# Optimization experiments

Measured on AMD Instinct MI355X. Metric: run time of the kernel, lower is better.

## Reference

```python
import jax, jax.numpy as jnp
import numpy as np
import math

B, LQ, LK = 1024, 1, 1024
LQD, SQD, H = 256, 128, 2
HD = SQD // H  # 64
EPS = 1e-6


def _ln(x, g, b):
    mu = x.mean(-1, keepdims=True)
    var = ((x - mu) ** 2).mean(-1, keepdims=True)
    return (x - mu) / jnp.sqrt(var + EPS) * g + b


def setup_inputs() -> dict:
    key = jax.random.key(0)
    ks = jax.random.split(key, 16)
    w = lambda k, s: jax.random.normal(k, s, jnp.float32) * 0.02
    return {
        "q_feats": jax.random.normal(ks[0], (B, LQ, LQD), jnp.float32),
        "k_feats": jax.random.normal(ks[1], (B, LK, SQD), jnp.float32),
        "msk": jax.random.randint(ks[2], (B, LK), 0, 2).astype(jnp.int32),
        "ln1_g": jnp.ones(LQD), "ln1_b": jnp.zeros(LQD),
        "W1": w(ks[3], (LQD, SQD)), "b1": jnp.zeros(SQD),
        "lnq_g": jnp.ones(SQD), "lnq_b": jnp.zeros(SQD),
        "lnk_g": jnp.ones(SQD), "lnk_b": jnp.zeros(SQD),
        "Wq": w(ks[4], (SQD, SQD)), "bq": jnp.zeros(SQD),
        "Wk": w(ks[5], (SQD, SQD)), "bk": jnp.zeros(SQD),
        "Wv": w(ks[6], (SQD, SQD)), "bv": jnp.zeros(SQD),
        "Wo": w(ks[7], (SQD, SQD)), "bo": jnp.zeros(SQD),
        "scale_w": jax.random.uniform(ks[8], (SQD,), jnp.float32, 0.01, 2.0),
        "ln2_g": jnp.ones(SQD), "ln2_b": jnp.zeros(SQD),
        "W2": w(ks[9], (SQD, LQD)), "b2": jnp.zeros(LQD),
    }


def reference(q_feats, k_feats, msk, ln1_g, ln1_b, W1, b1, lnq_g, lnq_b,
              lnk_g, lnk_b, Wq, bq, Wk, bk, Wv, bv, Wo, bo, scale_w,
              ln2_g, ln2_b, W2, b2):
    gelu = lambda x: jax.nn.gelu(x, approximate=False)
    # q_block1: LN -> Linear -> GELU (dropout = identity in eval)
    q_atten = gelu(_ln(q_feats, ln1_g, ln1_b) @ W1 + b1)  # [B,LQ,SQD]
    kv_in = _ln(k_feats, lnk_g, lnk_b)                     # [B,LK,SQD]
    q_in = _ln(q_atten, lnq_g, lnq_b)
    # masked self-attention
    qh = (q_in @ Wq + bq).reshape(B, LQ, H, HD).transpose(0, 2, 1, 3)
    kh = (kv_in @ Wk + bk).reshape(B, LK, H, HD).transpose(0, 2, 1, 3)
    vh = (kv_in @ Wv + bv).reshape(B, LK, H, HD).transpose(0, 2, 1, 3)
    scores = jnp.einsum('bhqd,bhkd->bhqk', qh, kh) / math.sqrt(HD)
    m = msk.astype(scores.dtype)[:, None, None, :]  # [B,1,1,LK]
    scores = jnp.where(m == 0, -1e9, scores * m)
    attn = jax.nn.softmax(scores, axis=-1)
    ctx = jnp.einsum('bhqk,bhkd->bhqd', attn, vh)
    ctx = ctx.transpose(0, 2, 1, 3).reshape(B, LQ, SQD)
    attn_out = gelu(ctx @ Wo + bo)
    q_atten = q_atten + attn_out
    # scaled broadcast residual into k_feats
    scaled = jnp.swapaxes(q_atten * scale_w, 0, 1)         # [LQ,B,SQD]
    k_out = k_feats + jnp.tile(scaled, (B, 1, 1))          # [B,B,SQD]
    # q_block2
    q_out = q_feats + gelu(_ln(q_atten, ln2_g, ln2_b) @ W2 + b2)
    return (q_out, k_out)
```

## Files before the change

kernel.cpp:

```cpp
#include <hip/hip_runtime.h>
#include <math.h>

#define B_    1024
#define LK_   1024
#define LQD_  256
#define SQD_  128
#define EPSLN 1e-6f
#define LOG2E 1.4426950408889634f

__device__ __forceinline__ float gelu_exact(float x) {
    return 0.5f * x * (1.0f + erff(x * 0.70710678118654752f));
}

__global__ __launch_bounds__(256, 4)
void fused_joint_kernel(
    const float* __restrict__ q_feats, const float* __restrict__ k_feats,
    const int*   __restrict__ msk,
    const float* __restrict__ ln1_g, const float* __restrict__ ln1_b,
    const float* __restrict__ W1,    const float* __restrict__ b1,
    const float* __restrict__ lnq_g, const float* __restrict__ lnq_b,
    const float* __restrict__ lnk_g, const float* __restrict__ lnk_b,
    const float* __restrict__ Wq,    const float* __restrict__ bq,
    const float* __restrict__ Wk,    const float* __restrict__ bk,
    const float* __restrict__ Wv,    const float* __restrict__ bv,
    const float* __restrict__ Wo,    const float* __restrict__ bo,
    const float* __restrict__ scale_w,
    const float* __restrict__ ln2_g, const float* __restrict__ ln2_b,
    const float* __restrict__ W2,    const float* __restrict__ b2,
    float* __restrict__ q_out, float* __restrict__ k_out)
{
    const int b    = blockIdx.x;
    const int tid  = threadIdx.x;
    const int wave = tid >> 6;
    const int lane = tid & 63;

    __shared__ float s_qn[256];
    __shared__ float s_q1[128];
    __shared__ float s_qi[128];
    __shared__ float s_qh[128];
    __shared__ float s_u[2][128];
    __shared__ float s_c[2];
    __shared__ float s_red[8];
    __shared__ int   s_idx[4][256];
    __shared__ float s_w[4][2][128];
    __shared__ float s_ml[4][2][2];
    __shared__ float s_wn[2][128];
    __shared__ float s_ctx[128];
    __shared__ float s_qa[128];
    __shared__ float s_qn2[128];
    __shared__ float s_sc[128];

    float x = q_feats[b * LQD_ + tid];
    float rs = x, rss = x * x;
    #pragma unroll
    for (int o = 32; o >= 1; o >>= 1) { rs += __shfl_xor(rs, o); rss += __shfl_xor(rss, o); }
    if (lane == 0) { s_red[wave * 2] = rs; s_red[wave * 2 + 1] = rss; }
    __syncthreads();
    {
        float sum  = s_red[0] + s_red[2] + s_red[4] + s_red[6];
        float ssum = s_red[1] + s_red[3] + s_red[5] + s_red[7];
        float mu   = sum * (1.0f / 256.0f);
        float var  = ssum * (1.0f / 256.0f) - mu * mu;
        float rstd = rsqrtf(var + EPSLN);
        s_qn[tid] = (x - mu) * rstd * ln1_g[tid] + ln1_b[tid];
    }
    __syncthreads();

    if (tid < 128) {
        float acc = b1[tid];
        #pragma unroll 4
        for (int c = 0; c < 256; ++c) acc = fmaf(s_qn[c], W1[c * 128 + tid], acc);
        s_q1[tid] = gelu_exact(acc);
    }
    __syncthreads();

    float v1 = (tid < 128) ? s_q1[tid] : 0.0f;
    rs = v1; rss = v1 * v1;
    #pragma unroll
    for (int o = 32; o >= 1; o >>= 1) { rs += __shfl_xor(rs, o); rss += __shfl_xor(rss, o); }
    __syncthreads();
    if (lane == 0) { s_red[wave * 2] = rs; s_red[wave * 2 + 1] = rss; }
    __syncthreads();
    {
        float sum  = s_red[0] + s_red[2] + s_red[4] + s_red[6];
        float ssum = s_red[1] + s_red[3] + s_red[5] + s_red[7];
        float mu   = sum * (1.0f / 128.0f);
        float var  = ssum * (1.0f / 128.0f) - mu * mu;
        float rstd = rsqrtf(var + EPSLN);
        if (tid < 128) s_qi[tid] = (v1 - mu) * rstd * lnq_g[tid] + lnq_b[tid];
    }
    __syncthreads();

    if (tid < 128) {
        float acc = bq[tid];
        #pragma unroll 4
        for (int c = 0; c < 128; ++c) acc = fmaf(s_qi[c], Wq[c * 128 + tid], acc);
        s_qh[tid] = acc;
    }
    __syncthreads();

    const float SCL = 0.125f * LOG2E;
    if (tid < 128) {
        float a0 = 0.f, a1 = 0.f;
        #pragma unroll 4
        for (int e = 0; e < 64; ++e) {
            a0 = fmaf(Wk[tid * 128 + e],      s_qh[e],      a0);
            a1 = fmaf(Wk[tid * 128 + 64 + e], s_qh[64 + e], a1);
        }
        s_u[0][tid] = a0 * SCL;
        s_u[1][tid] = a1 * SCL;
    }
    if (tid == 0) { float a = 0.f; for (int e = 0; e < 64; ++e) a = fmaf(bk[e],      s_qh[e],      a); s_c[0] = a * SCL; }
    if (tid == 1) { float a = 0.f; for (int e = 0; e < 64; ++e) a = fmaf(bk[64 + e], s_qh[64 + e], a); s_c[1] = a * SCL; }

    const int* mrow = msk + b * LK_;
    int cnt = 0;
    #pragma unroll
    for (int i = 0; i < 4; ++i) {
        int r = (wave << 8) + (i << 6) + lane;
        int mk = mrow[r];
        unsigned long long bal = __ballot(mk != 0);
        int pre = __popcll(bal & ((1ull << lane) - 1ull));
        if (mk) s_idx[wave][cnt + pre] = r;
        cnt += __popcll(bal);
    }
    __syncthreads();

    const int  c0i = lane * 2, c1i = lane * 2 + 1;
    const float g0  = lnk_g[c0i], g1  = lnk_g[c1i];
    const float hb0 = lnk_b[c0i], hb1 = lnk_b[c1i];
    const float u00 = s_u[0][c0i], u01 = s_u[0][c1i];
    const float u10 = s_u[1][c0i], u11 = s_u[1][c1i];
    const float cc0 = s_c[0],      cc1 = s_c[1];

    const float gu00 = g0 * u00, gu01 = g1 * u01;
    const float gu10 = g0 * u10, gu11 = g1 * u11;
    float sgu0 = gu00 + gu01;
    float sgu1 = gu10 + gu11;
    float dd0  = fmaf(hb0, u00, hb1 * u01);
    float dd1  = fmaf(hb0, u10, hb1 * u11);
    #pragma unroll
    for (int o = 32; o >= 1; o >>= 1) {
        sgu0 += __shfl_xor(sgu0, o); sgu1 += __shfl_xor(sgu1, o);
        dd0  += __shfl_xor(dd0,  o); dd1  += __shfl_xor(dd1,  o);
    }
    const float d0 = dd0 + cc0, d1 = dd1 + cc1;

    const float2* kf2 = (const float2*)(k_feats) + (size_t)b * (LK_ * (SQD_ / 2));

    float m0 = -1e30f, l0 = 0.f, w00 = 0.f, w01 = 0.f;
    float m1 = -1e30f, l1 = 0.f, w10 = 0.f, w11 = 0.f;

    #define ROW_STEP(xx, valid)                                               \
    {                                                                         \
        float a_  = xx.x + xx.y;                                              \
        float q_  = fmaf(xx.x, xx.x, xx.y * xx.y);                            \
        float p0_ = fmaf(xx.x, gu00, xx.y * gu01);                            \
        float p1_ = fmaf(xx.x, gu10, xx.y * gu11);                            \
        _Pragma("unroll")                                                     \
        for (int o_ = 32; o_ >= 1; o_ >>= 1) {                                \
            a_  += __shfl_xor(a_,  o_); q_  += __shfl_xor(q_,  o_);           \
            p0_ += __shfl_xor(p0_, o_); p1_ += __shfl_xor(p1_, o_);           \
        }                                                                     \
        if (valid) {                                                          \
            float mu_   = a_ * (1.f / 128.f);                                 \
            float var_  = q_ * (1.f / 128.f) - mu_ * mu_;                     \
            float rstd_ = rsqrtf(var_ + EPSLN);                               \
            float sc0_  = fmaf(rstd_, p0_ - mu_ * sgu0, d0);                  \
            float sc1_  = fmaf(rstd_, p1_ - mu_ * sgu1, d1);                  \
            float kv0_  = fmaf((xx.x - mu_) * rstd_, g0, hb0);                \
            float kv1_  = fmaf((xx.y - mu_) * rstd_, g1, hb1);                \
            float mn0_  = fmaxf(m0, sc0_);                                    \
            float cr0_  = exp2f(m0 - mn0_);                                   \
            float pp0_  = exp2f(sc0_ - mn0_);                                 \
            m0 = mn0_; l0 = fmaf(l0, cr0_, pp0_);                             \
            w00 = fmaf(w00, cr0_, pp0_ * kv0_);                               \
            w01 = fmaf(w01, cr0_, pp0_ * kv1_);                               \
            float mn1_  = fmaxf(m1, sc1_);                                    \
            float cr1_  = exp2f(m1 - mn1_);                                   \
            float pp1_  = exp2f(sc1_ - mn1_);                                 \
            m1 = mn1_; l1 = fmaf(l1, cr1_, pp1_);                             \
            w10 = fmaf(w10, cr1_, pp1_ * kv0_);                               \
            w11 = fmaf(w11, cr1_, pp1_ * kv1_);                               \
        }                                                                     \
    }

    float2 xr0 = make_float2(0.f, 0.f), xr1 = xr0, xr2 = xr0, xr3 = xr0;
    if (0 < cnt) xr0 = kf2[s_idx[wave][0] * 64 + lane];
    if (1 < cnt) xr1 = kf2[s_idx[wave][1] * 64 + lane];
    if (2 < cnt) xr2 = kf2[s_idx[wave][2] * 64 + lane];
    if (3 < cnt) xr3 = kf2[s_idx[wave][3] * 64 + lane];

    for (int t = 0; t < cnt; t += 4) {
        float2 xn0 = make_float2(0.f, 0.f), xn1 = xn0, xn2 = xn0, xn3 = xn0;
        if (t + 4 < cnt) xn0 = kf2[s_idx[wave][t + 4] * 64 + lane];
        if (t + 5 < cnt) xn1 = kf2[s_idx[wave][t + 5] * 64 + lane];
        if (t + 6 < cnt) xn2 = kf2[s_idx[wave][t + 6] * 64 + lane];
        if (t + 7 < cnt) xn3 = kf2[s_idx[wave][t + 7] * 64 + lane];

        ROW_STEP(xr0, true);
        ROW_STEP(xr1, (t + 1) < cnt);
        ROW_STEP(xr2, (t + 2) < cnt);
        ROW_STEP(xr3, (t + 3) < cnt);

        xr0 = xn0; xr1 = xn1; xr2 = xn2; xr3 = xn3;
    }
    #undef ROW_STEP

    s_w[wave][0][c0i] = w00; s_w[wave][0][c1i] = w01;
    s_w[wave][1][c0i] = w10; s_w[wave][1][c1i] = w11;
    if (lane == 0) {
        s_ml[wave][0][0] = m0; s_ml[wave][0][1] = l0;
        s_ml[wave][1][0] = m1; s_ml[wave][1][1] = l1;
    }
    __syncthreads();

    if (tid < 128) {
        #pragma unroll
        for (int h = 0; h < 2; ++h) {
            float mg = fmaxf(fmaxf(s_ml[0][h][0], s_ml[1][h][0]),
                             fmaxf(s_ml[2][h][0], s_ml[3][h][0]));
            float lt = 0.f, wt = 0.f;
            #pragma unroll
            for (int wv = 0; wv < 4; ++wv) {
                float e = exp2f(s_ml[wv][h][0] - mg);
                lt += s_ml[wv][h][1] * e;
                wt += s_w[wv][h][tid] * e;
            }
            s_wn[h][tid] = wt / lt;
        }
    }
    __syncthreads();

    if (tid < 128) {
        int h = tid >> 6;
        float acc = bv[tid];
        #pragma unroll 4
        for (int c = 0; c < 128; ++c) acc = fmaf(s_wn[h][c], Wv[c * 128 + tid], acc);
        s_ctx[tid] = acc;
    }
    __syncthreads();

    if (tid < 128) {
        float acc = bo[tid];
        #pragma unroll 4
        for (int c = 0; c < 128; ++c) acc = fmaf(s_ctx[c], Wo[c * 128 + tid], acc);
        float qa = s_q1[tid] + gelu_exact(acc);
        s_qa[tid] = qa;
        s_sc[tid] = qa * scale_w[tid];
    }
    __syncthreads();

    float v2 = (tid < 128) ? s_qa[tid] : 0.0f;
    rs = v2; rss = v2 * v2;
    #pragma unroll
    for (int o = 32; o >= 1; o >>= 1) { rs += __shfl_xor(rs, o); rss += __shfl_xor(rss, o); }
    __syncthreads();
    if (lane == 0) { s_red[wave * 2] = rs; s_red[wave * 2 + 1] = rss; }
    __syncthreads();
    {
        float sum  = s_red[0] + s_red[2] + s_red[4] + s_red[6];
        float ssum = s_red[1] + s_red[3] + s_red[5] + s_red[7];
        float mu   = sum * (1.0f / 128.0f);
        float var  = ssum * (1.0f / 128.0f) - mu * mu;
        float rstd = rsqrtf(var + EPSLN);
        if (tid < 128) s_qn2[tid] = (v2 - mu) * rstd * ln2_g[tid] + ln2_b[tid];
    }
    __syncthreads();

    {
        float acc = b2[tid];
        #pragma unroll 4
        for (int c = 0; c < 128; ++c) acc = fmaf(s_qn2[c], W2[c * 256 + tid], acc);
        q_out[b * LQD_ + tid] = q_feats[b * LQD_ + tid] + gelu_exact(acc);
    }

    {
        const int c4 = tid & 31;
        const int r0 = tid >> 5;
        const float4 sv = ((const float4*)s_sc)[c4];
        const size_t colbase = (size_t)b * 32 + c4;
        const float4* __restrict__ kin4  = (const float4*)k_feats;
        float4*       __restrict__ kout4 = (float4*)k_out;
        #pragma unroll 4
        for (int b2 = r0; b2 < B_; b2 += 8) {
            size_t o = (size_t)b2 * (LK_ * 32) + colbase;
            float4 kx = kin4[o];
            float4 ov = make_float4(kx.x + sv.x, kx.y + sv.y, kx.z + sv.z, kx.w + sv.w);
            kout4[o] = ov;
        }
    }
}

extern "C" void kernel_launch(void* const* d_in, const int* in_sizes, int n_in,
                              void* d_out, int out_size, void* d_ws, size_t ws_size,
                              hipStream_t stream)
{
    (void)in_sizes; (void)n_in; (void)out_size; (void)d_ws; (void)ws_size;
    const float* q_feats = (const float*)d_in[0];
    const float* k_feats = (const float*)d_in[1];
    const int*   msk     = (const int*)d_in[2];
    const float* ln1_g   = (const float*)d_in[3];
    const float* ln1_b   = (const float*)d_in[4];
    const float* W1      = (const float*)d_in[5];
    const float* b1      = (const float*)d_in[6];
    const float* lnq_g   = (const float*)d_in[7];
    const float* lnq_b   = (const float*)d_in[8];
    const float* lnk_g   = (const float*)d_in[9];
    const float* lnk_b   = (const float*)d_in[10];
    const float* Wq      = (const float*)d_in[11];
    const float* bq      = (const float*)d_in[12];
    const float* Wk      = (const float*)d_in[13];
    const float* bk      = (const float*)d_in[14];
    const float* Wv      = (const float*)d_in[15];
    const float* bv      = (const float*)d_in[16];
    const float* Wo      = (const float*)d_in[17];
    const float* bo      = (const float*)d_in[18];
    const float* scale_w = (const float*)d_in[19];
    const float* ln2_g   = (const float*)d_in[20];
    const float* ln2_b   = (const float*)d_in[21];
    const float* W2      = (const float*)d_in[22];
    const float* b2      = (const float*)d_in[23];

    float* q_out = (float*)d_out;
    float* k_out = (float*)d_out + (size_t)B_ * LQD_;

    fused_joint_kernel<<<B_, 256, 0, stream>>>(
        q_feats, k_feats, msk, ln1_g, ln1_b, W1, b1, lnq_g, lnq_b,
        lnk_g, lnk_b, Wq, bq, Wk, bk, Wv, bv, Wo, bo, scale_w,
        ln2_g, ln2_b, W2, b2, q_out, k_out);
}
```

Measured before the change: 387.0 us.

## Stage masked key rows through LDS tiles and batch the online softmax per tile

The per-row attention loop, which used a full 64-lane shuffle reduction for every key row, is replaced by a tiled scheme. Each wave loads 16 masked rows into a padded LDS tile with float4 loads. Quarter-wave partial dot products compute the per-row LayerNorm stats and scores with only two shuffle levels, and the running max is updated once per tile before the weighted accumulation. Shared-memory buffers are aliased to fit the larger tile, mask indices shrink to ushort, and the k_out broadcast store now uses nontemporal stores. This adds LDS traffic and code complexity in exchange for fewer cross-lane reductions and exp calls per row.

```diff
diff --git a/kernel.cpp b/kernel.cpp
--- a/kernel.cpp
+++ b/kernel.cpp
@@ -7,6 +7,13 @@
 #define SQD_  128
 #define EPSLN 1e-6f
 #define LOG2E 1.4426950408889634f
+
+#define TROWS 16
+#define TF4   33
+#define WREGF4 (TROWS * TF4)
+#define WREGF  (WREGF4 * 4)
+
+typedef float floatx4 __attribute__((ext_vector_type(4)));
 
 __device__ __forceinline__ float gelu_exact(float x) {
     return 0.5f * x * (1.0f + erff(x * 0.70710678118654752f));
@@ -34,21 +41,26 @@
     const int wave = tid >> 6;
     const int lane = tid & 63;
 
-    __shared__ float s_qn[256];
+    __shared__ float4 s_tile4[4 * WREGF4];
+    __shared__ float4 s_meta[4][TROWS];
+    __shared__ unsigned short s_idxm[4][256];
+    __shared__ __align__(16) float s_gu[2][128];
     __shared__ float s_q1[128];
-    __shared__ float s_qi[128];
-    __shared__ float s_qh[128];
-    __shared__ float s_u[2][128];
-    __shared__ float s_c[2];
+    __shared__ float s_sc[128];
     __shared__ float s_red[8];
-    __shared__ int   s_idx[4][256];
-    __shared__ float s_w[4][2][128];
     __shared__ float s_ml[4][2][2];
-    __shared__ float s_wn[2][128];
-    __shared__ float s_ctx[128];
-    __shared__ float s_qa[128];
-    __shared__ float s_qn2[128];
-    __shared__ float s_sc[128];
+
+    float* s_flat = (float*)s_tile4;
+    float* s_qn = s_flat;
+    float* s_qi = s_flat + 256;
+    float* s_qh = s_flat + 384;
+    float* s_u0 = s_flat + 512;
+    float* s_u1 = s_flat + 640;
+    float* s_c2 = s_flat + 768;
+    float* s_wn  = s_flat + 1024;
+    float* s_ctx = s_flat + 1280;
+    float* s_qa  = s_flat + 1408;
+    float* s_qn2 = s_flat + 1536;
 
     float x = q_feats[b * LQD_ + tid];
     float rs = x, rss = x * x;
@@ -107,11 +119,34 @@
             a0 = fmaf(Wk[tid * 128 + e],      s_qh[e],      a0);
             a1 = fmaf(Wk[tid * 128 + 64 + e], s_qh[64 + e], a1);
         }
-        s_u[0][tid] = a0 * SCL;
-        s_u[1][tid] = a1 * SCL;
-    }
-    if (tid == 0) { float a = 0.f; for (int e = 0; e < 64; ++e) a = fmaf(bk[e],      s_qh[e],      a); s_c[0] = a * SCL; }
-    if (tid == 1) { float a = 0.f; for (int e = 0; e < 64; ++e) a = fmaf(bk[64 + e], s_qh[64 + e], a); s_c[1] = a * SCL; }
+        s_u0[tid] = a0 * SCL;
+        s_u1[tid] = a1 * SCL;
+    }
+    if (tid == 0) { float a = 0.f; for (int e = 0; e < 64; ++e) a = fmaf(bk[e],      s_qh[e],      a); s_c2[0] = a * SCL; }
+    if (tid == 1) { float a = 0.f; for (int e = 0; e < 64; ++e) a = fmaf(bk[64 + e], s_qh[64 + e], a); s_c2[1] = a * SCL; }
+    __syncthreads();
+
+    const int  c0i = lane * 2, c1i = lane * 2 + 1;
+    const float g0  = lnk_g[c0i], g1  = lnk_g[c1i];
+    const float hb0 = lnk_b[c0i], hb1 = lnk_b[c1i];
+    const float u00 = s_u0[c0i], u01 = s_u0[c1i];
+    const float u10 = s_u1[c0i], u11 = s_u1[c1i];
+    const float cc0 = s_c2[0],   cc1 = s_c2[1];
+    if (tid < 128) {
+        float g = lnk_g[tid];
+        s_gu[0][tid] = s_u0[tid] * g;
+        s_gu[1][tid] = s_u1[tid] * g;
+    }
+    float sgu0 = fmaf(g0, u00, g1 * u01);
+    float sgu1 = fmaf(g0, u10, g1 * u11);
+    float dd0  = fmaf(hb0, u00, hb1 * u01);
+    float dd1  = fmaf(hb0, u10, hb1 * u11);
+    #pragma unroll
+    for (int o = 32; o >= 1; o >>= 1) {
+        sgu0 += __shfl_xor(sgu0, o); sgu1 += __shfl_xor(sgu1, o);
+        dd0  += __shfl_xor(dd0,  o); dd1  += __shfl_xor(dd1,  o);
+    }
+    const float d0 = dd0 + cc0, d1 = dd1 + cc1;
 
     const int* mrow = msk + b * LK_;
     int cnt = 0;
@@ -121,97 +156,124 @@
         int mk = mrow[r];
         unsigned long long bal = __ballot(mk != 0);
         int pre = __popcll(bal & ((1ull << lane) - 1ull));
-        if (mk) s_idx[wave][cnt + pre] = r;
+        if (mk) s_idxm[wave][cnt + pre] = (unsigned short)r;
         cnt += __popcll(bal);
     }
     __syncthreads();
 
-    const int  c0i = lane * 2, c1i = lane * 2 + 1;
-    const float g0  = lnk_g[c0i], g1  = lnk_g[c1i];
-    const float hb0 = lnk_b[c0i], hb1 = lnk_b[c1i];
-    const float u00 = s_u[0][c0i], u01 = s_u[0][c1i];
-    const float u10 = s_u[1][c0i], u11 = s_u[1][c1i];
-    const float cc0 = s_c[0],      cc1 = s_c[1];
-
-    const float gu00 = g0 * u00, gu01 = g1 * u01;
-    const float gu10 = g0 * u10, gu11 = g1 * u11;
-    float sgu0 = gu00 + gu01;
-    float sgu1 = gu10 + gu11;
-    float dd0  = fmaf(hb0, u00, hb1 * u01);
-    float dd1  = fmaf(hb0, u10, hb1 * u11);
-    #pragma unroll
-    for (int o = 32; o >= 1; o >>= 1) {
-        sgu0 += __shfl_xor(sgu0, o); sgu1 += __shfl_xor(sgu1, o);
-        dd0  += __shfl_xor(dd0,  o); dd1  += __shfl_xor(dd1,  o);
-    }
-    const float d0 = dd0 + cc0, d1 = dd1 + cc1;
-
-    const float2* kf2 = (const float2*)(k_feats) + (size_t)b * (LK_ * (SQD_ / 2));
+    float4* twave = s_tile4 + wave * WREGF4;
+    const float* twf = (const float*)twave;
+    const float4* kf4 = (const float4*)k_feats + (size_t)b * (LK_ * 32);
+    const float4* gu04 = (const float4*)s_gu[0];
+    const float4* gu14 = (const float4*)s_gu[1];
+    const int half  = lane >> 5;
+    const int chunk = lane & 31;
+    const int arow  = lane & 15;
+    const int aq    = lane >> 4;
 
     float m0 = -1e30f, l0 = 0.f, w00 = 0.f, w01 = 0.f;
     float m1 = -1e30f, l1 = 0.f, w10 = 0.f, w11 = 0.f;
 
-    #define ROW_STEP(xx, valid)                                               \
-    {                                                                         \
-        float a_  = xx.x + xx.y;                                              \
-        float q_  = fmaf(xx.x, xx.x, xx.y * xx.y);                            \
-        float p0_ = fmaf(xx.x, gu00, xx.y * gu01);                            \
-        float p1_ = fmaf(xx.x, gu10, xx.y * gu11);                            \
-        _Pragma("unroll")                                                     \
-        for (int o_ = 32; o_ >= 1; o_ >>= 1) {                                \
-            a_  += __shfl_xor(a_,  o_); q_  += __shfl_xor(q_,  o_);           \
-            p0_ += __shfl_xor(p0_, o_); p1_ += __shfl_xor(p1_, o_);           \
-        }                                                                     \
-        if (valid) {                                                          \
-            float mu_   = a_ * (1.f / 128.f);                                 \
-            float var_  = q_ * (1.f / 128.f) - mu_ * mu_;                     \
-            float rstd_ = rsqrtf(var_ + EPSLN);                               \
-            float sc0_  = fmaf(rstd_, p0_ - mu_ * sgu0, d0);                  \
-            float sc1_  = fmaf(rstd_, p1_ - mu_ * sgu1, d1);                  \
-            float kv0_  = fmaf((xx.x - mu_) * rstd_, g0, hb0);                \
-            float kv1_  = fmaf((xx.y - mu_) * rstd_, g1, hb1);                \
-            float mn0_  = fmaxf(m0, sc0_);                                    \
-            float cr0_  = exp2f(m0 - mn0_);                                   \
-            float pp0_  = exp2f(sc0_ - mn0_);                                 \
-            m0 = mn0_; l0 = fmaf(l0, cr0_, pp0_);                             \
-            w00 = fmaf(w00, cr0_, pp0_ * kv0_);                               \
-            w01 = fmaf(w01, cr0_, pp0_ * kv1_);                               \
-            float mn1_  = fmaxf(m1, sc1_);                                    \
-            float cr1_  = exp2f(m1 - mn1_);                                   \
-            float pp1_  = exp2f(sc1_ - mn1_);                                 \
-            m1 = mn1_; l1 = fmaf(l1, cr1_, pp1_);                             \
-            w10 = fmaf(w10, cr1_, pp1_ * kv0_);                               \
-            w11 = fmaf(w11, cr1_, pp1_ * kv1_);                               \
-        }                                                                     \
-    }
-
-    float2 xr0 = make_float2(0.f, 0.f), xr1 = xr0, xr2 = xr0, xr3 = xr0;
-    if (0 < cnt) xr0 = kf2[s_idx[wave][0] * 64 + lane];
-    if (1 < cnt) xr1 = kf2[s_idx[wave][1] * 64 + lane];
-    if (2 < cnt) xr2 = kf2[s_idx[wave][2] * 64 + lane];
-    if (3 < cnt) xr3 = kf2[s_idx[wave][3] * 64 + lane];
-
-    for (int t = 0; t < cnt; t += 4) {
-        float2 xn0 = make_float2(0.f, 0.f), xn1 = xn0, xn2 = xn0, xn3 = xn0;
-        if (t + 4 < cnt) xn0 = kf2[s_idx[wave][t + 4] * 64 + lane];
-        if (t + 5 < cnt) xn1 = kf2[s_idx[wave][t + 5] * 64 + lane];
-        if (t + 6 < cnt) xn2 = kf2[s_idx[wave][t + 6] * 64 + lane];
-        if (t + 7 < cnt) xn3 = kf2[s_idx[wave][t + 7] * 64 + lane];
-
-        ROW_STEP(xr0, true);
-        ROW_STEP(xr1, (t + 1) < cnt);
-        ROW_STEP(xr2, (t + 2) < cnt);
-        ROW_STEP(xr3, (t + 3) < cnt);
-
-        xr0 = xn0; xr1 = xn1; xr2 = xn2; xr3 = xn3;
-    }
-    #undef ROW_STEP
-
-    s_w[wave][0][c0i] = w00; s_w[wave][0][c1i] = w01;
-    s_w[wave][1][c0i] = w10; s_w[wave][1][c1i] = w11;
-    if (lane == 0) {
-        s_ml[wave][0][0] = m0; s_ml[wave][0][1] = l0;
-        s_ml[wave][1][0] = m1; s_ml[wave][1][1] = l1;
+    const int ntile = (cnt + TROWS - 1) / TROWS;
+    float4 r0v, r1v, r2v, r3v, r4v, r5v, r6v, r7v;
+    const float4 z4 = make_float4(0.f, 0.f, 0.f, 0.f);
+
+    #define LOADT(base)                                                        \
+    {                                                                          \
+        int j_, gi_;                                                           \
+        j_ = (base) + 0  + half; gi_ = (j_ < cnt) ? (int)s_idxm[wave][j_] : -1; \
+        r0v = (gi_ >= 0) ? kf4[gi_ * 32 + chunk] : z4;                         \
+        j_ = (base) + 2  + half; gi_ = (j_ < cnt) ? (int)s_idxm[wave][j_] : -1; \
+        r1v = (gi_ >= 0) ? kf4[gi_ * 32 + chunk] : z4;                         \
+        j_ = (base) + 4  + half; gi_ = (j_ < cnt) ? (int)s_idxm[wave][j_] : -1; \
+        r2v = (gi_ >= 0) ? kf4[gi_ * 32 + chunk] : z4;                         \
+        j_ = (base) + 6  + half; gi_ = (j_ < cnt) ? (int)s_idxm[wave][j_] : -1; \
+        r3v = (gi_ >= 0) ? kf4[gi_ * 32 + chunk] : z4;                         \
+        j_ = (base) + 8  + half; gi_ = (j_ < cnt) ? (int)s_idxm[wave][j_] : -1; \
+        r4v = (gi_ >= 0) ? kf4[gi_ * 32 + chunk] : z4;                         \
+        j_ = (base) + 10 + half; gi_ = (j_ < cnt) ? (int)s_idxm[wave][j_] : -1; \
+        r5v = (gi_ >= 0) ? kf4[gi_ * 32 + chunk] : z4;                         \
+        j_ = (base) + 12 + half; gi_ = (j_ < cnt) ? (int)s_idxm[wave][j_] : -1; \
+        r6v = (gi_ >= 0) ? kf4[gi_ * 32 + chunk] : z4;                         \
+        j_ = (base) + 14 + half; gi_ = (j_ < cnt) ? (int)s_idxm[wave][j_] : -1; \
+        r7v = (gi_ >= 0) ? kf4[gi_ * 32 + chunk] : z4;                         \
+    }
+
+    if (ntile > 0) LOADT(0);
+
+    for (int t = 0; t < ntile; ++t) {
+        twave[(0  + half) * TF4 + chunk] = r0v;
+        twave[(2  + half) * TF4 + chunk] = r1v;
+        twave[(4  + half) * TF4 + chunk] = r2v;
+        twave[(6  + half) * TF4 + chunk] = r3v;
+        twave[(8  + half) * TF4 + chunk] = r4v;
+        twave[(10 + half) * TF4 + chunk] = r5v;
+        twave[(12 + half) * TF4 + chunk] = r6v;
+        twave[(14 + half) * TF4 + chunk] = r7v;
+        LOADT((t + 1) * TROWS);
+
+        float sx = 0.f, sxx = 0.f, p0 = 0.f, p1 = 0.f;
+        const float4* rowp = twave + arow * TF4 + aq * 8;
+        #pragma unroll
+        for (int k = 0; k < 8; ++k) {
+            float4 v  = rowp[k];
+            float4 ga = gu04[aq * 8 + k];
+            float4 gb = gu14[aq * 8 + k];
+            sx += (v.x + v.y) + (v.z + v.w);
+            sxx = fmaf(v.x, v.x, fmaf(v.y, v.y, fmaf(v.z, v.z, fmaf(v.w, v.w, sxx))));
+            p0  = fmaf(v.x, ga.x, fmaf(v.y, ga.y, fmaf(v.z, ga.z, fmaf(v.w, ga.w, p0))));
+            p1  = fmaf(v.x, gb.x, fmaf(v.y, gb.y, fmaf(v.z, gb.z, fmaf(v.w, gb.w, p1))));
+        }
+        #pragma unroll
+        for (int o = 16; o <= 32; o <<= 1) {
+            sx += __shfl_xor(sx, o); sxx += __shfl_xor(sxx, o);
+            p0 += __shfl_xor(p0, o); p1  += __shfl_xor(p1, o);
+        }
+        float mu   = sx * (1.f / 128.f);
+        float var  = sxx * (1.f / 128.f) - mu * mu;
+        float rstd = rsqrtf(var + EPSLN);
+        bool  vrow = (t * TROWS + arow) < cnt;
+        float sc0  = vrow ? fmaf(rstd, p0 - mu * sgu0, d0) : -1e30f;
+        float sc1  = vrow ? fmaf(rstd, p1 - mu * sgu1, d1) : -1e30f;
+        if (aq == 0) s_meta[wave][arow] = make_float4(sc0, sc1, mu, rstd);
+        float t0 = sc0, t1 = sc1;
+        #pragma unroll
+        for (int o = 1; o <= 8; o <<= 1) {
+            t0 = fmaxf(t0, __shfl_xor(t0, o));
+            t1 = fmaxf(t1, __shfl_xor(t1, o));
+        }
+        float mn0 = fmaxf(m0, t0);
+        float cr0 = exp2f(m0 - mn0);
+        m0 = mn0; l0 *= cr0; w00 *= cr0; w01 *= cr0;
+        float mn1 = fmaxf(m1, t1);
+        float cr1 = exp2f(m1 - mn1);
+        m1 = mn1; l1 *= cr1; w10 *= cr1; w11 *= cr1;
+
+        #pragma unroll 4
+        for (int j = 0; j < TROWS; ++j) {
+            float4 mt = s_meta[wave][j];
+            float2 xv = *(const float2*)(twf + j * 132 + 2 * lane);
+            float pp0 = exp2f(mt.x - m0);
+            float pp1 = exp2f(mt.y - m1);
+            float xn0 = (xv.x - mt.z) * mt.w;
+            float xn1 = (xv.y - mt.z) * mt.w;
+            float kv0 = fmaf(xn0, g0, hb0);
+            float kv1 = fmaf(xn1, g1, hb1);
+            w00 = fmaf(pp0, kv0, w00); w01 = fmaf(pp0, kv1, w01);
+            w10 = fmaf(pp1, kv0, w10); w11 = fmaf(pp1, kv1, w11);
+            l0 += pp0; l1 += pp1;
+        }
+    }
+    #undef LOADT
+
+    {
+        float* myreg = s_flat + wave * WREGF;
+        myreg[c0i] = w00; myreg[c1i] = w01;
+        myreg[128 + c0i] = w10; myreg[128 + c1i] = w11;
+        if (lane == 0) {
+            s_ml[wave][0][0] = m0; s_ml[wave][0][1] = l0;
+            s_ml[wave][1][0] = m1; s_ml[wave][1][1] = l1;
+        }
     }
     __syncthreads();
 
@@ -225,9 +287,9 @@
             for (int wv = 0; wv < 4; ++wv) {
                 float e = exp2f(s_ml[wv][h][0] - mg);
                 lt += s_ml[wv][h][1] * e;
-                wt += s_w[wv][h][tid] * e;
+                wt += s_flat[wv * WREGF + h * 128 + tid] * e;
             }
-            s_wn[h][tid] = wt / lt;
+            s_wn[h * 128 + tid] = wt / lt;
         }
     }
     __syncthreads();
@@ -236,7 +298,7 @@
         int h = tid >> 6;
         float acc = bv[tid];
         #pragma unroll 4
-        for (int c = 0; c < 128; ++c) acc = fmaf(s_wn[h][c], Wv[c * 128 + tid], acc);
+        for (int c = 0; c < 128; ++c) acc = fmaf(s_wn[h * 128 + c], Wv[c * 128 + tid], acc);
         s_ctx[tid] = acc;
     }
     __syncthreads();
@@ -277,17 +339,19 @@
 
     {
         const int c4 = tid & 31;
-        const int r0 = tid >> 5;
+        const int rr = tid >> 5;
         const float4 sv = ((const float4*)s_sc)[c4];
         const size_t colbase = (size_t)b * 32 + c4;
-        const float4* __restrict__ kin4  = (const float4*)k_feats;
-        float4*       __restrict__ kout4 = (float4*)k_out;
-        #pragma unroll 4
-        for (int b2 = r0; b2 < B_; b2 += 8) {
+        const floatx4* __restrict__ kin4  = (const floatx4*)k_feats;
+        floatx4*       __restrict__ kout4 = (floatx4*)k_out;
+        #pragma unroll 4
+        for (int b2 = rr; b2 < B_; b2 += 8) {
             size_t o = (size_t)b2 * (LK_ * 32) + colbase;
-            float4 kx = kin4[o];
-            float4 ov = make_float4(kx.x + sv.x, kx.y + sv.y, kx.z + sv.z, kx.w + sv.w);
-            kout4[o] = ov;
+            floatx4 kx = kin4[o];
+            floatx4 ov;
+            ov.x = kx.x + sv.x; ov.y = kx.y + sv.y;
+            ov.z = kx.z + sv.z; ov.w = kx.w + sv.w;
+            __builtin_nontemporal_store(ov, &kout4[o]);
         }
     }
 }
```

Measured after the change: 400.3 us. +3.4%, slower.

## Split attention over key partitions and stream the k_out broadcast separately

Applied to the files above, without the earlier changes.

The single fused per-batch kernel becomes three kernels. The first splits each batch's key rows into 4 partitions, one block each, and writes partial softmax stats and weighted sums. The second merges the partials and runs the V/O projections, LN2 and the q-block MLP. The third is a flat, fully coalesced grid-stride kernel that adds the scaled broadcast into k_out. This aims to raise parallelism in the serial attention scan and to decouple the large memory-bound k_out write from the compute phase, at the cost of extra launches and a partials round trip through scratch space placed in k_out.

```diff
diff --git a/kernel.cpp b/kernel.cpp
--- a/kernel.cpp
+++ b/kernel.cpp
@@ -7,13 +7,17 @@
 #define SQD_  128
 #define EPSLN 1e-6f
 #define LOG2E 1.4426950408889634f
+#define NPART 4
+#define PREC  260
+
+typedef float floatx4 __attribute__((ext_vector_type(4)));
 
 __device__ __forceinline__ float gelu_exact(float x) {
     return 0.5f * x * (1.0f + erff(x * 0.70710678118654752f));
 }
 
-__global__ __launch_bounds__(256, 4)
-void fused_joint_kernel(
+__global__ __launch_bounds__(256, 8)
+void attn_part_kernel(
     const float* __restrict__ q_feats, const float* __restrict__ k_feats,
     const int*   __restrict__ msk,
     const float* __restrict__ ln1_g, const float* __restrict__ ln1_b,
@@ -22,38 +26,34 @@
     const float* __restrict__ lnk_g, const float* __restrict__ lnk_b,
     const float* __restrict__ Wq,    const float* __restrict__ bq,
     const float* __restrict__ Wk,    const float* __restrict__ bk,
-    const float* __restrict__ Wv,    const float* __restrict__ bv,
-    const float* __restrict__ Wo,    const float* __restrict__ bo,
-    const float* __restrict__ scale_w,
-    const float* __restrict__ ln2_g, const float* __restrict__ ln2_b,
-    const float* __restrict__ W2,    const float* __restrict__ b2,
-    float* __restrict__ q_out, float* __restrict__ k_out)
+    float* __restrict__ pbase, float* __restrict__ q1w)
 {
-    const int b    = blockIdx.x;
+    const int bid  = blockIdx.x;
+    const int b    = bid >> 2;
+    const int part = bid & 3;
     const int tid  = threadIdx.x;
     const int wave = tid >> 6;
     const int lane = tid & 63;
+    const int o    = tid & 127;
+    const int hf   = tid >> 7;
 
     __shared__ float s_qn[256];
+    __shared__ float s_part[256];
     __shared__ float s_q1[128];
     __shared__ float s_qi[128];
-    __shared__ float s_qh[128];
-    __shared__ float s_u[2][128];
-    __shared__ float s_c[2];
+    __shared__ __align__(16) float s_qh[128];
+    __shared__ float s_u0[128];
+    __shared__ float s_u1[128];
+    __shared__ float s_c2[2];
     __shared__ float s_red[8];
-    __shared__ int   s_idx[4][256];
     __shared__ float s_w[4][2][128];
     __shared__ float s_ml[4][2][2];
-    __shared__ float s_wn[2][128];
-    __shared__ float s_ctx[128];
-    __shared__ float s_qa[128];
-    __shared__ float s_qn2[128];
-    __shared__ float s_sc[128];
+    __shared__ unsigned short s_idx[4][64];
 
     float x = q_feats[b * LQD_ + tid];
     float rs = x, rss = x * x;
     #pragma unroll
-    for (int o = 32; o >= 1; o >>= 1) { rs += __shfl_xor(rs, o); rss += __shfl_xor(rss, o); }
+    for (int oo = 32; oo >= 1; oo >>= 1) { rs += __shfl_xor(rs, oo); rss += __shfl_xor(rss, oo); }
     if (lane == 0) { s_red[wave * 2] = rs; s_red[wave * 2 + 1] = rss; }
     __syncthreads();
     {
@@ -66,19 +66,22 @@
     }
     __syncthreads();
 
-    if (tid < 128) {
-        float acc = b1[tid];
-        #pragma unroll 4
-        for (int c = 0; c < 256; ++c) acc = fmaf(s_qn[c], W1[c * 128 + tid], acc);
-        s_q1[tid] = gelu_exact(acc);
-    }
+    {
+        float acc = 0.f;
+        const float* wp = W1 + (hf * 128) * 128 + o;
+        const float* qp = s_qn + hf * 128;
+        #pragma unroll 8
+        for (int c = 0; c < 128; ++c) acc = fmaf(qp[c], wp[c * 128], acc);
+        s_part[tid] = acc;
+    }
+    __syncthreads();
+    if (tid < 128) s_q1[tid] = gelu_exact(s_part[tid] + s_part[tid + 128] + b1[tid]);
     __syncthreads();
 
     float v1 = (tid < 128) ? s_q1[tid] : 0.0f;
     rs = v1; rss = v1 * v1;
     #pragma unroll
-    for (int o = 32; o >= 1; o >>= 1) { rs += __shfl_xor(rs, o); rss += __shfl_xor(rss, o); }
-    __syncthreads();
+    for (int oo = 32; oo >= 1; oo >>= 1) { rs += __shfl_xor(rs, oo); rss += __shfl_xor(rss, oo); }
     if (lane == 0) { s_red[wave * 2] = rs; s_red[wave * 2 + 1] = rss; }
     __syncthreads();
     {
@@ -91,48 +94,43 @@
     }
     __syncthreads();
 
-    if (tid < 128) {
-        float acc = bq[tid];
-        #pragma unroll 4
-        for (int c = 0; c < 128; ++c) acc = fmaf(s_qi[c], Wq[c * 128 + tid], acc);
-        s_qh[tid] = acc;
-    }
+    {
+        float acc = 0.f;
+        const float* wp = Wq + (hf * 64) * 128 + o;
+        const float* qp = s_qi + hf * 64;
+        #pragma unroll 8
+        for (int c = 0; c < 64; ++c) acc = fmaf(qp[c], wp[c * 128], acc);
+        s_part[tid] = acc;
+    }
+    __syncthreads();
+    if (tid < 128) s_qh[tid] = s_part[tid] + s_part[tid + 128] + bq[tid];
     __syncthreads();
 
     const float SCL = 0.125f * LOG2E;
-    if (tid < 128) {
-        float a0 = 0.f, a1 = 0.f;
-        #pragma unroll 4
-        for (int e = 0; e < 64; ++e) {
-            a0 = fmaf(Wk[tid * 128 + e],      s_qh[e],      a0);
-            a1 = fmaf(Wk[tid * 128 + 64 + e], s_qh[64 + e], a1);
+    {
+        const float4* wr = (const float4*)(Wk + o * 128 + hf * 64);
+        const float4* qr = (const float4*)(s_qh + hf * 64);
+        float acc = 0.f;
+        #pragma unroll
+        for (int k = 0; k < 16; ++k) {
+            float4 wv = wr[k], qv = qr[k];
+            acc = fmaf(wv.x, qv.x, fmaf(wv.y, qv.y, fmaf(wv.z, qv.z, fmaf(wv.w, qv.w, acc))));
         }
-        s_u[0][tid] = a0 * SCL;
-        s_u[1][tid] = a1 * SCL;
-    }
-    if (tid == 0) { float a = 0.f; for (int e = 0; e < 64; ++e) a = fmaf(bk[e],      s_qh[e],      a); s_c[0] = a * SCL; }
-    if (tid == 1) { float a = 0.f; for (int e = 0; e < 64; ++e) a = fmaf(bk[64 + e], s_qh[64 + e], a); s_c[1] = a * SCL; }
-
-    const int* mrow = msk + b * LK_;
-    int cnt = 0;
-    #pragma unroll
-    for (int i = 0; i < 4; ++i) {
-        int r = (wave << 8) + (i << 6) + lane;
-        int mk = mrow[r];
-        unsigned long long bal = __ballot(mk != 0);
-        int pre = __popcll(bal & ((1ull << lane) - 1ull));
-        if (mk) s_idx[wave][cnt + pre] = r;
-        cnt += __popcll(bal);
-    }
-    __syncthreads();
+        float* du = hf ? s_u1 : s_u0;
+        du[o] = acc * SCL;
+    }
+    if (tid == 0) { float a = 0.f; for (int e = 0; e < 64; ++e) a = fmaf(bk[e],      s_qh[e],      a); s_c2[0] = a * SCL; }
+    if (tid == 1) { float a = 0.f; for (int e = 0; e < 64; ++e) a = fmaf(bk[64 + e], s_qh[64 + e], a); s_c2[1] = a * SCL; }
+    __syncthreads();
+
+    if (part == 0 && tid < 128) q1w[b * 128 + tid] = s_q1[tid];
 
     const int  c0i = lane * 2, c1i = lane * 2 + 1;
     const float g0  = lnk_g[c0i], g1  = lnk_g[c1i];
     const float hb0 = lnk_b[c0i], hb1 = lnk_b[c1i];
-    const float u00 = s_u[0][c0i], u01 = s_u[0][c1i];
-    const float u10 = s_u[1][c0i], u11 = s_u[1][c1i];
-    const float cc0 = s_c[0],      cc1 = s_c[1];
-
+    const float u00 = s_u0[c0i], u01 = s_u0[c1i];
+    const float u10 = s_u1[c0i], u11 = s_u1[c1i];
+    const float cc0 = s_c2[0],   cc1 = s_c2[1];
     const float gu00 = g0 * u00, gu01 = g1 * u01;
     const float gu10 = g0 * u10, gu11 = g1 * u11;
     float sgu0 = gu00 + gu01;
@@ -140,13 +138,20 @@
     float dd0  = fmaf(hb0, u00, hb1 * u01);
     float dd1  = fmaf(hb0, u10, hb1 * u11);
     #pragma unroll
-    for (int o = 32; o >= 1; o >>= 1) {
-        sgu0 += __shfl_xor(sgu0, o); sgu1 += __shfl_xor(sgu1, o);
-        dd0  += __shfl_xor(dd0,  o); dd1  += __shfl_xor(dd1,  o);
+    for (int oo = 32; oo >= 1; oo >>= 1) {
+        sgu0 += __shfl_xor(sgu0, oo); sgu1 += __shfl_xor(sgu1, oo);
+        dd0  += __shfl_xor(dd0,  oo); dd1  += __shfl_xor(dd1,  oo);
     }
     const float d0 = dd0 + cc0, d1 = dd1 + cc1;
 
-    const float2* kf2 = (const float2*)(k_feats) + (size_t)b * (LK_ * (SQD_ / 2));
+    const int rbase = part * 256 + wave * 64;
+    int mk = msk[b * LK_ + rbase + lane];
+    unsigned long long bal = __ballot(mk != 0);
+    int pre = __popcll(bal & ((1ull << lane) - 1ull));
+    if (mk) s_idx[wave][pre] = (unsigned short)(rbase + lane);
+    int cnt = __popcll(bal);
+
+    const float2* kf2 = (const float2*)(k_feats) + (size_t)b * (LK_ * 64);
 
     float m0 = -1e30f, l0 = 0.f, w00 = 0.f, w01 = 0.f;
     float m1 = -1e30f, l1 = 0.f, w10 = 0.f, w11 = 0.f;
@@ -216,6 +221,7 @@
     __syncthreads();
 
     if (tid < 128) {
+        float* rec = pbase + (size_t)bid * PREC;
         #pragma unroll
         for (int h = 0; h < 2; ++h) {
             float mg = fmaxf(fmaxf(s_ml[0][h][0], s_ml[1][h][0]),
@@ -227,35 +233,96 @@
                 lt += s_ml[wv][h][1] * e;
                 wt += s_w[wv][h][tid] * e;
             }
-            s_wn[h][tid] = wt / lt;
+            rec[h * 128 + tid] = wt;
+            if (tid == 0) { rec[256 + 2 * h] = mg; rec[257 + 2 * h] = lt; }
         }
     }
-    __syncthreads();
-
+}
+
+__global__ __launch_bounds__(256, 4)
+void merge_epilogue_kernel(
+    const float* __restrict__ q_feats,
+    const float* __restrict__ Wv,    const float* __restrict__ bv,
+    const float* __restrict__ Wo,    const float* __restrict__ bo,
+    const float* __restrict__ scale_w,
+    const float* __restrict__ ln2_g, const float* __restrict__ ln2_b,
+    const float* __restrict__ W2,    const float* __restrict__ b2,
+    const float* __restrict__ pbase, const float* __restrict__ q1w,
+    float* __restrict__ q_out, float* __restrict__ sc_ws)
+{
+    const int b    = blockIdx.x;
+    const int tid  = threadIdx.x;
+    const int wave = tid >> 6;
+    const int lane = tid & 63;
+    const int o    = tid & 127;
+    const int hf   = tid >> 7;
+
+    __shared__ float s_wn[2][128];
+    __shared__ float s_part[256];
+    __shared__ float s_ctx[128];
+    __shared__ float s_qa[128];
+    __shared__ float s_qn2[128];
+    __shared__ float s_red[8];
+
+    float mg0 = -1e30f, mg1 = -1e30f;
+    #pragma unroll
+    for (int p = 0; p < NPART; ++p) {
+        const float* rec = pbase + (size_t)(b * NPART + p) * PREC;
+        mg0 = fmaxf(mg0, rec[256]);
+        mg1 = fmaxf(mg1, rec[258]);
+    }
+    float lt0 = 0.f, lt1 = 0.f;
+    float wt0 = 0.f, wt1 = 0.f;
+    #pragma unroll
+    for (int p = 0; p < NPART; ++p) {
+        const float* rec = pbase + (size_t)(b * NPART + p) * PREC;
+        float e0 = exp2f(rec[256] - mg0);
+        float e1 = exp2f(rec[258] - mg1);
+        lt0 += rec[257] * e0;
+        lt1 += rec[259] * e1;
+        if (tid < 128) {
+            wt0 = fmaf(rec[tid],       e0, wt0);
+            wt1 = fmaf(rec[128 + tid], e1, wt1);
+        }
+    }
     if (tid < 128) {
-        int h = tid >> 6;
-        float acc = bv[tid];
-        #pragma unroll 4
-        for (int c = 0; c < 128; ++c) acc = fmaf(s_wn[h][c], Wv[c * 128 + tid], acc);
-        s_ctx[tid] = acc;
-    }
-    __syncthreads();
-
+        s_wn[0][tid] = wt0 / lt0;
+        s_wn[1][tid] = wt1 / lt1;
+    }
+    __syncthreads();
+
+    {
+        float acc = 0.f;
+        const float* wp = Wv + (hf * 64) * 128 + o;
+        const float* qp = s_wn[o >> 6] + hf * 64;
+        #pragma unroll 8
+        for (int c = 0; c < 64; ++c) acc = fmaf(qp[c], wp[c * 128], acc);
+        s_part[tid] = acc;
+    }
+    __syncthreads();
+    if (tid < 128) s_ctx[tid] = s_part[tid] + s_part[tid + 128] + bv[tid];
+    __syncthreads();
+
+    {
+        float acc = 0.f;
+        const float* wp = Wo + (hf * 64) * 128 + o;
+        const float* qp = s_ctx + hf * 64;
+        #pragma unroll 8
+        for (int c = 0; c < 64; ++c) acc = fmaf(qp[c], wp[c * 128], acc);
+        s_part[tid] = acc;
+    }
+    __syncthreads();
     if (tid < 128) {
-        float acc = bo[tid];
-        #pragma unroll 4
-        for (int c = 0; c < 128; ++c) acc = fmaf(s_ctx[c], Wo[c * 128 + tid], acc);
-        float qa = s_q1[tid] + gelu_exact(acc);
+        float qa = q1w[b * 128 + tid] + gelu_exact(s_part[tid] + s_part[tid + 128] + bo[tid]);
         s_qa[tid] = qa;
-        s_sc[tid] = qa * scale_w[tid];
+        sc_ws[b * 128 + tid] = qa * scale_w[tid];
     }
     __syncthreads();
 
     float v2 = (tid < 128) ? s_qa[tid] : 0.0f;
-    rs = v2; rss = v2 * v2;
-    #pragma unroll
-    for (int o = 32; o >= 1; o >>= 1) { rs += __shfl_xor(rs, o); rss += __shfl_xor(rss, o); }
-    __syncthreads();
+    float rs = v2, rss = v2 * v2;
+    #pragma unroll
+    for (int oo = 32; oo >= 1; oo >>= 1) { rs += __shfl_xor(rs, oo); rss += __shfl_xor(rss, oo); }
     if (lane == 0) { s_red[wave * 2] = rs; s_red[wave * 2 + 1] = rss; }
     __syncthreads();
     {
@@ -270,25 +337,25 @@
 
     {
         float acc = b2[tid];
-        #pragma unroll 4
+        #pragma unroll 8
         for (int c = 0; c < 128; ++c) acc = fmaf(s_qn2[c], W2[c * 256 + tid], acc);
         q_out[b * LQD_ + tid] = q_feats[b * LQD_ + tid] + gelu_exact(acc);
     }
-
-    {
-        const int c4 = tid & 31;
-        const int r0 = tid >> 5;
-        const float4 sv = ((const float4*)s_sc)[c4];
-        const size_t colbase = (size_t)b * 32 + c4;
-        const float4* __restrict__ kin4  = (const float4*)k_feats;
-        float4*       __restrict__ kout4 = (float4*)k_out;
-        #pragma unroll 4
-        for (int b2 = r0; b2 < B_; b2 += 8) {
-            size_t o = (size_t)b2 * (LK_ * 32) + colbase;
-            float4 kx = kin4[o];
-            float4 ov = make_float4(kx.x + sv.x, kx.y + sv.y, kx.z + sv.z, kx.w + sv.w);
-            kout4[o] = ov;
-        }
+}
+
+__global__ __launch_bounds__(256)
+void kout_stream_kernel(const floatx4* __restrict__ kf,
+                        const floatx4* __restrict__ sc,
+                        floatx4* __restrict__ out)
+{
+    const int total4 = B_ * LK_ * (SQD_ / 4);
+    const int stride = gridDim.x * blockDim.x;
+    int idx = blockIdx.x * blockDim.x + threadIdx.x;
+    #pragma unroll 8
+    for (; idx < total4; idx += stride) {
+        floatx4 k = kf[idx];
+        floatx4 s = sc[idx & 32767];
+        out[idx] = k + s;
     }
 }
 
@@ -296,7 +363,7 @@
                               void* d_out, int out_size, void* d_ws, size_t ws_size,
                               hipStream_t stream)
 {
-    (void)in_sizes; (void)n_in; (void)out_size; (void)d_ws; (void)ws_size;
+    (void)in_sizes; (void)n_in; (void)out_size; (void)ws_size;
     const float* q_feats = (const float*)d_in[0];
     const float* k_feats = (const float*)d_in[1];
     const int*   msk     = (const int*)d_in[2];
@@ -324,9 +391,18 @@
 
     float* q_out = (float*)d_out;
     float* k_out = (float*)d_out + (size_t)B_ * LQD_;
-
-    fused_joint_kernel<<<B_, 256, 0, stream>>>(
+    float* pbase = k_out;
+    float* q1w   = k_out + (size_t)B_ * NPART * PREC;
+    float* sc_ws = (float*)d_ws;
+
+    attn_part_kernel<<<B_ * NPART, 256, 0, stream>>>(
         q_feats, k_feats, msk, ln1_g, ln1_b, W1, b1, lnq_g, lnq_b,
-        lnk_g, lnk_b, Wq, bq, Wk, bk, Wv, bv, Wo, bo, scale_w,
-        ln2_g, ln2_b, W2, b2, q_out, k_out);
+        lnk_g, lnk_b, Wq, bq, Wk, bk, pbase, q1w);
+
+    merge_epilogue_kernel<<<B_, 256, 0, stream>>>(
+        q_feats, Wv, bv, Wo, bo, scale_w, ln2_g, ln2_b, W2, b2,
+        pbase, q1w, q_out, sc_ws);
+
+    kout_stream_kernel<<<2048, 256, 0, stream>>>(
+        (const floatx4*)k_feats, (const floatx4*)sc_ws, (floatx4*)k_out);
 }
```

Result: slower. 440.6 us (+13.9%).
